# Kernel tuning notes

Measured on AMD Instinct MI355X. Metric: run time of the kernel, lower is better.

The kernel has to match this reference:

```python
import jax, jax.numpy as jnp
import numpy as np

B, N, C, H, E, K = 2, 2048, 1024, 4096, 8, 2
TAU = 1.0


def setup_inputs() -> dict:
    key = jax.random.key(0)
    ks = jax.random.split(key, 9)
    x = jax.random.normal(ks[0], (B, N, C), dtype=jnp.float32)
    T = B * N
    u = jax.random.uniform(ks[1], (T, E), minval=1e-6, maxval=1.0 - 1e-6)
    gumbel_noise = -jnp.log(-jnp.log(u))  # Gumbel(0,1) samples
    s = 0.02
    gate_w = jax.random.normal(ks[2], (C, E), dtype=jnp.float32) * s
    gate_b = jnp.zeros((E,), dtype=jnp.float32)
    w1 = jax.random.normal(ks[3], (E, C, H), dtype=jnp.float32) * s
    b1 = jnp.zeros((E, H), dtype=jnp.float32)
    w2 = jax.random.normal(ks[4], (E, H, C), dtype=jnp.float32) * s
    b2 = jnp.zeros((E, C), dtype=jnp.float32)
    return {"x": x, "gumbel_noise": gumbel_noise, "gate_w": gate_w,
            "gate_b": gate_b, "w1": w1, "b1": b1, "w2": w2, "b2": b2}


def reference(x, gumbel_noise, gate_w, gate_b, w1, b1, w2, b2):
    Bb, Nn, Cc = x.shape
    x_flat = x.reshape(-1, Cc)                                  # [T, C]
    logits = x_flat @ gate_w + gate_b                           # [T, E]
    # F.gumbel_softmax(hard=False, tau=1): softmax((logits + g)/tau)
    gates = jax.nn.softmax((logits + gumbel_noise) / TAU, axis=-1)
    mean_gates = gates.mean(axis=0)
    load_balance_loss = jnp.sum(mean_gates * jnp.log(mean_gates + 1e-8))
    topk_vals, topk_idxs = jax.lax.top_k(gates, K)              # [T, K]
    T = x_flat.shape[0]
    # scatter top-k gate weights into a dense [T, E] combine matrix
    comb = jnp.zeros((T, E), dtype=gates.dtype)
    comb = comb.at[jnp.arange(T)[:, None], topk_idxs].set(topk_vals)
    # dense per-expert MLP over all tokens, then weighted combine
    h = jnp.einsum('tc,ech->teh', x_flat, w1) + b1              # [T, E, H]
    h = jax.nn.gelu(h, approximate=False)                        # exact GELU (nn.GELU)
    y = jnp.einsum('teh,ehc->tec', h, w2) + b2                  # [T, E, C]
    out = jnp.einsum('te,tec->tc', comb, y)                     # [T, C]
    return out.reshape(Bb, Nn, Cc), load_balance_loss
```

## Files before the change

### kernel.cpp

```cpp
#include <hip/hip_runtime.h>
#include <math.h>

#define TT  4096
#define CC  1024
#define HH  4096
#define EE  8
#define TKN 8192

typedef _Float16 f16x8 __attribute__((ext_vector_type(8)));
typedef float    f32x4 __attribute__((ext_vector_type(4)));

#define GLD_LDS16(g, l)                                                        \
    __builtin_amdgcn_global_load_lds(                                          \
        (const __attribute__((address_space(1))) void*)(g),                    \
        (__attribute__((address_space(3))) void*)(l), 16, 0, 0)

__global__ __launch_bounds__(256) void gate_kernel(
    const float* __restrict__ x, const float* __restrict__ gn,
    const float* __restrict__ gw, const float* __restrict__ gb,
    int* __restrict__ topk_idx, float* __restrict__ topk_w,
    int* __restrict__ counts, float* __restrict__ gsum)
{
    int wave = threadIdx.x >> 6, lane = threadIdx.x & 63;
    int t = blockIdx.x * 4 + wave;
    const float* xrow = x + (size_t)t * CC;

    double acc[EE];
#pragma unroll
    for (int e = 0; e < EE; e++) acc[e] = 0.0;

#pragma unroll
    for (int i = 0; i < CC / 64; i++) {
        int c = i * 64 + lane;
        float xv = xrow[c];
        const float4* g4 = reinterpret_cast<const float4*>(gw + (size_t)c * EE);
        float4 g0 = g4[0], g1 = g4[1];
        double xd = (double)xv;
        acc[0] += xd * (double)g0.x; acc[1] += xd * (double)g0.y;
        acc[2] += xd * (double)g0.z; acc[3] += xd * (double)g0.w;
        acc[4] += xd * (double)g1.x; acc[5] += xd * (double)g1.y;
        acc[6] += xd * (double)g1.z; acc[7] += xd * (double)g1.w;
    }
#pragma unroll
    for (int e = 0; e < EE; e++)
#pragma unroll
        for (int off = 32; off > 0; off >>= 1)
            acc[e] += __shfl_xor(acc[e], off);

    double z[EE], m = -1e300;
#pragma unroll
    for (int e = 0; e < EE; e++) {
        z[e] = acc[e] + (double)gb[e] + (double)gn[(size_t)t * EE + e];
        m = fmax(m, z[e]);
    }
    double p[EE], s = 0.0;
#pragma unroll
    for (int e = 0; e < EE; e++) { p[e] = exp(z[e] - m); s += p[e]; }
    double inv = 1.0 / s;
    double g[EE];
#pragma unroll
    for (int e = 0; e < EE; e++) g[e] = p[e] * inv;

    int i1 = 0; double v1 = g[0];
#pragma unroll
    for (int e = 1; e < EE; e++) if (g[e] > v1) { v1 = g[e]; i1 = e; }
    int i2 = -1; double v2 = -1.0;
#pragma unroll
    for (int e = 0; e < EE; e++) if (e != i1 && g[e] > v2) { v2 = g[e]; i2 = e; }

    if (lane == 0) {
        topk_idx[t * 2 + 0] = i1; topk_w[t * 2 + 0] = (float)v1;
        topk_idx[t * 2 + 1] = i2; topk_w[t * 2 + 1] = (float)v2;
        atomicAdd(&counts[i1], 1);
        atomicAdd(&counts[i2], 1);
    }

    __shared__ float gp[4][EE];
    if (lane == 0) {
#pragma unroll
        for (int e = 0; e < EE; e++) gp[wave][e] = (float)g[e];
    }
    __syncthreads();
    if (threadIdx.x < EE) {
        float s4 = gp[0][threadIdx.x] + gp[1][threadIdx.x] +
                   gp[2][threadIdx.x] + gp[3][threadIdx.x];
        atomicAdd(&gsum[threadIdx.x], s4);
    }
}

__global__ __launch_bounds__(256) void transpose_f16_kernel(
    const float* __restrict__ src, _Float16* __restrict__ dst, int R, int Ccols)
{
    __shared__ float tile[64][65];
    int e = blockIdx.z;
    const float* s = src + (size_t)e * R * Ccols;
    _Float16* d = dst + (size_t)e * R * Ccols;
    int c0 = blockIdx.x * 64, r0 = blockIdx.y * 64;
    int tid = threadIdx.x;

    int lr = tid >> 4;
    int lc = (tid & 15) * 4;
#pragma unroll
    for (int i = 0; i < 4; i++) {
        int r = lr + i * 16;
        float4 v = *reinterpret_cast<const float4*>(
            s + (size_t)(r0 + r) * Ccols + c0 + lc);
        tile[r][lc + 0] = v.x; tile[r][lc + 1] = v.y;
        tile[r][lc + 2] = v.z; tile[r][lc + 3] = v.w;
    }
    __syncthreads();

    int oc = tid >> 2;
    int orr = (tid & 3) * 16;
    f16x8 o0, o1;
#pragma unroll
    for (int j = 0; j < 8; j++) o0[j] = (_Float16)tile[orr + j][oc];
#pragma unroll
    for (int j = 0; j < 8; j++) o1[j] = (_Float16)tile[orr + 8 + j][oc];
    *reinterpret_cast<f16x8*>(d + (size_t)(c0 + oc) * R + r0 + orr)     = o0;
    *reinterpret_cast<f16x8*>(d + (size_t)(c0 + oc) * R + r0 + orr + 8) = o1;
}

__global__ void scan_kernel(const int* __restrict__ counts, int* __restrict__ offsets,
                            const float* __restrict__ gsum, float* __restrict__ loss_out)
{
    if (threadIdx.x == 0) {
        int o = 0;
#pragma unroll
        for (int e = 0; e < EE; e++) { offsets[e] = o; o += counts[e]; }
        offsets[EE] = o;
        float L = 0.f;
#pragma unroll
        for (int e = 0; e < EE; e++) {
            float me = gsum[e] / (float)TT;
            L += me * logf(me + 1e-8f);
        }
        *loss_out = L;
    }
}

__global__ __launch_bounds__(256) void scatter_kernel(
    const int* __restrict__ topk_idx, const int* __restrict__ offsets,
    int* __restrict__ fill, int* __restrict__ rowtok, int* __restrict__ posmap)
{
    int t = blockIdx.x * 256 + threadIdx.x;
#pragma unroll
    for (int k = 0; k < 2; k++) {
        int e = topk_idx[t * 2 + k];
        int pos = offsets[e] + atomicAdd(&fill[e], 1);
        rowtok[pos] = t;
        posmap[t * 2 + k] = pos;
    }
}

__global__ __launch_bounds__(256) void gather_kernel(
    const float* __restrict__ x, const int* __restrict__ rowtok,
    _Float16* __restrict__ xg)
{
    int p = blockIdx.x * 2 + (threadIdx.x >> 7);
    int c = (threadIdx.x & 127) * 8;
    int t = rowtok[p];
    const float4* s = reinterpret_cast<const float4*>(x + (size_t)t * CC + c);
    float4 v0 = s[0], v1 = s[1];
    f16x8 o;
    o[0] = (_Float16)v0.x; o[1] = (_Float16)v0.y;
    o[2] = (_Float16)v0.z; o[3] = (_Float16)v0.w;
    o[4] = (_Float16)v1.x; o[5] = (_Float16)v1.y;
    o[6] = (_Float16)v1.z; o[7] = (_Float16)v1.w;
    *reinterpret_cast<f16x8*>(xg + (size_t)p * CC + c) = o;
}


__global__ __launch_bounds__(512, 2) void gemm1_kernel(
    const _Float16* __restrict__ xg, const _Float16* __restrict__ w1t,
    const float* __restrict__ b1, const int* __restrict__ offsets,
    _Float16* __restrict__ h)
{
    int GX = gridDim.x, GY = gridDim.y;
    int nwg = GX * GY * (int)gridDim.z;
    int f = blockIdx.x + GX * (blockIdx.y + GY * blockIdx.z);
    int cpx = nwg >> 3;
    f = (f & 7) * cpx + (f >> 3);
    int bx = f % GX; int tq = f / GX; int by = tq % GY; int bz = tq / GY;

    int e = bz;
    int segs = offsets[e];
    int M = offsets[e + 1] - segs;
    int m0 = bx * 256;
    if (m0 >= M) return;
    int n0 = by * 256;

    __shared__ __align__(16) _Float16 As[2][256 * 64];
    __shared__ __align__(16) _Float16 Bs[2][256 * 64];

    int tid = threadIdx.x;
    int wave = tid >> 6, lane = tid & 63;
    int wm = (wave >> 2) * 128, wn = (wave & 3) * 64;
    int lrow = lane & 15, kg = lane >> 4;
    int rx = lrow & 7;

    const _Float16* wB = w1t + (size_t)e * HH * CC;

    const _Float16* ap[4]; const _Float16* bp[4];
    int lofs[4];
#pragma unroll
    for (int j = 0; j < 4; j++) {
        int ch = j * 512 + tid;
        int row = ch >> 3, slot = ch & 7;
        int col = ((slot ^ (row & 7)) * 8);
        int rm = m0 + row; if (rm >= M) rm = M - 1;
        ap[j] = xg + (size_t)(segs + rm) * CC + col;
        bp[j] = wB + (size_t)(n0 + row) * CC + col;
        lofs[j] = ch * 8;
    }

    f32x4 acc[8][4];
#pragma unroll
    for (int i = 0; i < 8; i++)
#pragma unroll
        for (int j = 0; j < 4; j++)
#pragma unroll
            for (int q = 0; q < 4; q++) acc[i][j][q] = 0.f;

    auto STAGE = [&](int b) {
#pragma unroll
        for (int j = 0; j < 4; j++) {
            GLD_LDS16(ap[j], &As[b][0] + lofs[j]);
            GLD_LDS16(bp[j], &Bs[b][0] + lofs[j]);
            ap[j] += 64; bp[j] += 64;
        }
    };

    const int NK = CC / 64;
    STAGE(0);
    __syncthreads();
    int cur = 0;
    for (int t = 0; t < NK; ++t) {
        if (t + 1 < NK) STAGE(cur ^ 1);
        const _Float16* Ab = &As[cur][0];
        const _Float16* Bb = &Bs[cur][0];
#pragma unroll
        for (int s = 0; s < 2; s++) {
            f16x8 aF[8], bF[4];
#pragma unroll
            for (int i = 0; i < 8; i++) {
                int row = wm + i * 16 + lrow;
                aF[i] = *reinterpret_cast<const f16x8*>(
                    Ab + row * 64 + (((s * 4 + kg) ^ rx) * 8));
            }
#pragma unroll
            for (int j = 0; j < 4; j++) {
                int row = wn + j * 16 + lrow;
                bF[j] = *reinterpret_cast<const f16x8*>(
                    Bb + row * 64 + (((s * 4 + kg) ^ rx) * 8));
            }
            __builtin_amdgcn_s_setprio(1);
#pragma unroll
            for (int i = 0; i < 8; i++)
#pragma unroll
                for (int j = 0; j < 4; j++)
                    acc[i][j] = __builtin_amdgcn_mfma_f32_16x16x32_f16(
                        aF[i], bF[j], acc[i][j], 0, 0, 0);
            __builtin_amdgcn_s_setprio(0);
        }
        __syncthreads();
        cur ^= 1;
    }

    int rbase = (lane >> 4) * 4;
#pragma unroll
    for (int mi = 0; mi < 8; mi++) {
#pragma unroll
        for (int ni = 0; ni < 4; ni++) {
            int gcol = n0 + wn + ni * 16 + lrow;
            float bias = b1[(size_t)e * HH + gcol];
#pragma unroll
            for (int q = 0; q < 4; q++) {
                int rowl = m0 + wm + mi * 16 + rbase + q;
                if (rowl < M) {
                    float v = acc[mi][ni][q] + bias;
                    v = 0.5f * v * (1.0f + erff(v * 0.70710678118654752f));
                    h[(size_t)(segs + rowl) * HH + gcol] = (_Float16)v;
                }
            }
        }
    }
}

__global__ __launch_bounds__(512, 2) void gemm2_kernel(
    const _Float16* __restrict__ h, const _Float16* __restrict__ w2t,
    const float* __restrict__ b2, const int* __restrict__ offsets,
    float* __restrict__ y)
{
    int GX = gridDim.x, GY = gridDim.y;
    int nwg = GX * GY * (int)gridDim.z;
    int f = blockIdx.x + GX * (blockIdx.y + GY * blockIdx.z);
    int cpx = nwg >> 3;
    f = (f & 7) * cpx + (f >> 3);
    int bx = f % GX; int tq = f / GX; int by = tq % GY; int bz = tq / GY;

    int e = bz;
    int segs = offsets[e];
    int M = offsets[e + 1] - segs;
    int m0 = bx * 256;
    if (m0 >= M) return;
    int kz = by >> 2;
    int n0 = (by & 3) * 256;
    int kbeg = kz * (HH / 2);

    __shared__ __align__(16) _Float16 As[2][256 * 64];
    __shared__ __align__(16) _Float16 Bs[2][256 * 64];

    int tid = threadIdx.x;
    int wave = tid >> 6, lane = tid & 63;
    int wm = (wave >> 2) * 128, wn = (wave & 3) * 64;
    int lrow = lane & 15, kg = lane >> 4;
    int rx = lrow & 7;

    const _Float16* wB = w2t + (size_t)e * CC * HH;

    const _Float16* ap[4]; const _Float16* bp[4];
    int lofs[4];
#pragma unroll
    for (int j = 0; j < 4; j++) {
        int ch = j * 512 + tid;
        int row = ch >> 3, slot = ch & 7;
        int col = ((slot ^ (row & 7)) * 8);
        int rm = m0 + row; if (rm >= M) rm = M - 1;
        ap[j] = h  + (size_t)(segs + rm) * HH + kbeg + col;
        bp[j] = wB + (size_t)(n0 + row) * HH + kbeg + col;
        lofs[j] = ch * 8;
    }

    f32x4 acc[8][4];
#pragma unroll
    for (int i = 0; i < 8; i++)
#pragma unroll
        for (int j = 0; j < 4; j++)
#pragma unroll
            for (int q = 0; q < 4; q++) acc[i][j][q] = 0.f;

    auto STAGE = [&](int b) {
#pragma unroll
        for (int j = 0; j < 4; j++) {
            GLD_LDS16(ap[j], &As[b][0] + lofs[j]);
            GLD_LDS16(bp[j], &Bs[b][0] + lofs[j]);
            ap[j] += 64; bp[j] += 64;
        }
    };

    const int NK = (HH / 2) / 64;
    STAGE(0);
    __syncthreads();
    int cur = 0;
    for (int t = 0; t < NK; ++t) {
        if (t + 1 < NK) STAGE(cur ^ 1);
        const _Float16* Ab = &As[cur][0];
        const _Float16* Bb = &Bs[cur][0];
#pragma unroll
        for (int s = 0; s < 2; s++) {
            f16x8 aF[8], bF[4];
#pragma unroll
            for (int i = 0; i < 8; i++) {
                int row = wm + i * 16 + lrow;
                aF[i] = *reinterpret_cast<const f16x8*>(
                    Ab + row * 64 + (((s * 4 + kg) ^ rx) * 8));
            }
#pragma unroll
            for (int j = 0; j < 4; j++) {
                int row = wn + j * 16 + lrow;
                bF[j] = *reinterpret_cast<const f16x8*>(
                    Bb + row * 64 + (((s * 4 + kg) ^ rx) * 8));
            }
            __builtin_amdgcn_s_setprio(1);
#pragma unroll
            for (int i = 0; i < 8; i++)
#pragma unroll
                for (int j = 0; j < 4; j++)
                    acc[i][j] = __builtin_amdgcn_mfma_f32_16x16x32_f16(
                        aF[i], bF[j], acc[i][j], 0, 0, 0);
            __builtin_amdgcn_s_setprio(0);
        }
        __syncthreads();
        cur ^= 1;
    }

    float* yk = y + (size_t)kz * TKN * CC;
    int rbase = (lane >> 4) * 4;
#pragma unroll
    for (int mi = 0; mi < 8; mi++) {
#pragma unroll
        for (int ni = 0; ni < 4; ni++) {
            int gcol = n0 + wn + ni * 16 + lrow;
            float bias = (kz == 0) ? b2[(size_t)e * CC + gcol] : 0.f;
#pragma unroll
            for (int q = 0; q < 4; q++) {
                int rowl = m0 + wm + mi * 16 + rbase + q;
                if (rowl < M)
                    yk[(size_t)(segs + rowl) * CC + gcol] = acc[mi][ni][q] + bias;
            }
        }
    }
}

__global__ __launch_bounds__(256) void combine_kernel(
    const float* __restrict__ y, const int* __restrict__ posmap,
    const float* __restrict__ topk_w, float* __restrict__ out)
{
    int t = blockIdx.x * 2 + (threadIdx.x >> 7);
    int c = (threadIdx.x & 127) * 8;
    int p0 = posmap[t * 2 + 0], p1 = posmap[t * 2 + 1];
    float wa = topk_w[t * 2 + 0], wb = topk_w[t * 2 + 1];
    const float* y1 = y + (size_t)TKN * CC;
    const float4* a0 = reinterpret_cast<const float4*>(y  + (size_t)p0 * CC + c);
    const float4* a1 = reinterpret_cast<const float4*>(y1 + (size_t)p0 * CC + c);
    const float4* b0 = reinterpret_cast<const float4*>(y  + (size_t)p1 * CC + c);
    const float4* b1 = reinterpret_cast<const float4*>(y1 + (size_t)p1 * CC + c);
    float4 r0, r1;
    float4 av0 = a0[0], av1 = a0[1], aw0 = a1[0], aw1 = a1[1];
    float4 bv0 = b0[0], bv1 = b0[1], bw0 = b1[0], bw1 = b1[1];
    r0.x = wa * (av0.x + aw0.x) + wb * (bv0.x + bw0.x);
    r0.y = wa * (av0.y + aw0.y) + wb * (bv0.y + bw0.y);
    r0.z = wa * (av0.z + aw0.z) + wb * (bv0.z + bw0.z);
    r0.w = wa * (av0.w + aw0.w) + wb * (bv0.w + bw0.w);
    r1.x = wa * (av1.x + aw1.x) + wb * (bv1.x + bw1.x);
    r1.y = wa * (av1.y + aw1.y) + wb * (bv1.y + bw1.y);
    r1.z = wa * (av1.z + aw1.z) + wb * (bv1.z + bw1.z);
    r1.w = wa * (av1.w + aw1.w) + wb * (bv1.w + bw1.w);
    float4* o = reinterpret_cast<float4*>(out + (size_t)t * CC + c);
    o[0] = r0; o[1] = r1;
}

extern "C" void kernel_launch(void* const* d_in, const int* in_sizes, int n_in,
                              void* d_out, int out_size, void* d_ws, size_t ws_size,
                              hipStream_t stream)
{
    const float* x  = (const float*)d_in[0];
    const float* gn = (const float*)d_in[1];
    const float* gw = (const float*)d_in[2];
    const float* gb = (const float*)d_in[3];
    const float* w1 = (const float*)d_in[4];
    const float* b1 = (const float*)d_in[5];
    const float* w2 = (const float*)d_in[6];
    const float* b2 = (const float*)d_in[7];
    float* out = (float*)d_out;

    char* w = (char*)d_ws;
    int*   counts  = (int*)(w + 0);
    int*   fill    = (int*)(w + 32);
    int*   offsets = (int*)(w + 64);
    float* gsum    = (float*)(w + 128);
    size_t off = 256;
    int*   topk_idx = (int*)(w + off);   off += (size_t)TT * 2 * 4;
    float* topk_w   = (float*)(w + off); off += (size_t)TT * 2 * 4;
    int*   rowtok   = (int*)(w + off);   off += (size_t)TKN * 4;
    int*   posmap   = (int*)(w + off);   off += (size_t)TKN * 4;
    _Float16* xg  = (_Float16*)(w + off); off += (size_t)TKN * CC * 2;
    _Float16* w1t = (_Float16*)(w + off); off += (size_t)EE * HH * CC * 2;
    _Float16* w2t = (_Float16*)(w + off); off += (size_t)EE * CC * HH * 2;
    _Float16* hbuf = (_Float16*)(w + off); off += (size_t)TKN * HH * 2;
    float* ybuf = (float*)w1t;

    (void)hipMemsetAsync(d_ws, 0, 256, stream);

    gate_kernel<<<TT / 4, 256, 0, stream>>>(x, gn, gw, gb, topk_idx, topk_w,
                                            counts, gsum);
    transpose_f16_kernel<<<dim3(HH / 64, CC / 64, EE), 256, 0, stream>>>(
        w1, w1t, CC, HH);
    transpose_f16_kernel<<<dim3(CC / 64, HH / 64, EE), 256, 0, stream>>>(
        w2, w2t, HH, CC);
    scan_kernel<<<1, 64, 0, stream>>>(counts, offsets, gsum, out + (size_t)TT * CC);
    scatter_kernel<<<TT / 256, 256, 0, stream>>>(topk_idx, offsets, fill,
                                                 rowtok, posmap);
    gather_kernel<<<TKN / 2, 256, 0, stream>>>(x, rowtok, xg);
    gemm1_kernel<<<dim3(6, HH / 256, EE), 512, 0, stream>>>(xg, w1t, b1,
                                                            offsets, hbuf);
    gemm2_kernel<<<dim3(6, 2 * (CC / 256), EE), 512, 0, stream>>>(
        hbuf, w2t, b2, offsets, ybuf);
    combine_kernel<<<TT / 2, 256, 0, stream>>>(ybuf, posmap, topk_w, out);
}
```

Baseline: 848.1 us.

## Shrink GEMM tiles to 128x128, drop gemm2 split-K, fuse weight transposes

Both expert GEMMs move from 256x256 tiles with 512 threads to 128x128 tiles with 256 threads. The grid is doubled in M so it still covers the largest expert, which improves load balance across ragged expert sizes. Gemm2 drops its 2-way split-K, so the combine kernel reads one y buffer instead of summing two partial buffers. The two weight transpose launches become a single kernel in which each block handles four 64x64 tiles, loading the next tile while storing the current one. Smaller tiles lower arithmetic intensity and increase global and LDS traffic per FLOP.

Measured after the change: 882.8 us. 4.1% more time.

```diff
diff --git a/kernel.cpp b/kernel.cpp
--- a/kernel.cpp
+++ b/kernel.cpp
@@ -88,37 +88,63 @@
     }
 }
 
-__global__ __launch_bounds__(256) void transpose_f16_kernel(
-    const float* __restrict__ src, _Float16* __restrict__ dst, int R, int Ccols)
-{
-    __shared__ float tile[64][65];
-    int e = blockIdx.z;
-    const float* s = src + (size_t)e * R * Ccols;
-    _Float16* d = dst + (size_t)e * R * Ccols;
-    int c0 = blockIdx.x * 64, r0 = blockIdx.y * 64;
+__global__ __launch_bounds__(256) void transpose_both_kernel(
+    const float* __restrict__ w1, _Float16* __restrict__ w1t,
+    const float* __restrict__ w2, _Float16* __restrict__ w2t)
+{
+    __shared__ float tile[2][64][65];
+    int idx = blockIdx.x;
+    const float* src; _Float16* dst; int R, Cc, localn;
+    if (idx < 2048) { src = w1; dst = w1t; R = CC; Cc = HH; localn = idx; }
+    else            { src = w2; dst = w2t; R = HH; Cc = CC; localn = idx - 2048; }
+    int e = localn >> 8;
+    int rem = localn & 255;
+    int ctiles = Cc >> 8;
+    int ct = rem % ctiles, rt = rem / ctiles;
+    int c0 = ct * 256, r0 = rt * 64;
+    src += (size_t)e * R * Cc;
+    dst += (size_t)e * R * Cc;
+
     int tid = threadIdx.x;
-
     int lr = tid >> 4;
     int lc = (tid & 15) * 4;
-#pragma unroll
-    for (int i = 0; i < 4; i++) {
-        int r = lr + i * 16;
-        float4 v = *reinterpret_cast<const float4*>(
-            s + (size_t)(r0 + r) * Ccols + c0 + lc);
-        tile[r][lc + 0] = v.x; tile[r][lc + 1] = v.y;
-        tile[r][lc + 2] = v.z; tile[r][lc + 3] = v.w;
-    }
-    __syncthreads();
-
     int oc = tid >> 2;
     int orr = (tid & 3) * 16;
-    f16x8 o0, o1;
-#pragma unroll
-    for (int j = 0; j < 8; j++) o0[j] = (_Float16)tile[orr + j][oc];
-#pragma unroll
-    for (int j = 0; j < 8; j++) o1[j] = (_Float16)tile[orr + 8 + j][oc];
-    *reinterpret_cast<f16x8*>(d + (size_t)(c0 + oc) * R + r0 + orr)     = o0;
-    *reinterpret_cast<f16x8*>(d + (size_t)(c0 + oc) * R + r0 + orr + 8) = o1;
+
+    float4 v[4];
+    auto GLOAD = [&](int t) {
+#pragma unroll
+        for (int i = 0; i < 4; i++)
+            v[i] = *reinterpret_cast<const float4*>(
+                src + (size_t)(r0 + lr + i * 16) * Cc + c0 + t * 64 + lc);
+    };
+    auto LWRITE = [&](int b) {
+#pragma unroll
+        for (int i = 0; i < 4; i++) {
+            tile[b][lr + i * 16][lc + 0] = v[i].x;
+            tile[b][lr + i * 16][lc + 1] = v[i].y;
+            tile[b][lr + i * 16][lc + 2] = v[i].z;
+            tile[b][lr + i * 16][lc + 3] = v[i].w;
+        }
+    };
+    auto STORE = [&](int t, int b) {
+        f16x8 o0, o1;
+#pragma unroll
+        for (int j = 0; j < 8; j++) o0[j] = (_Float16)tile[b][orr + j][oc];
+#pragma unroll
+        for (int j = 0; j < 8; j++) o1[j] = (_Float16)tile[b][orr + 8 + j][oc];
+        _Float16* dp = dst + (size_t)(c0 + t * 64 + oc) * R + r0 + orr;
+        *reinterpret_cast<f16x8*>(dp)     = o0;
+        *reinterpret_cast<f16x8*>(dp + 8) = o1;
+    };
+
+    GLOAD(0); LWRITE(0);
+    for (int t = 0; t < 4; ++t) {
+        __syncthreads();
+        if (t < 3) GLOAD(t + 1);
+        STORE(t, t & 1);
+        if (t < 3) LWRITE((t + 1) & 1);
+    }
 }
 
 __global__ void scan_kernel(const int* __restrict__ counts, int* __restrict__ offsets,
@@ -171,7 +197,7 @@
 }
 
 
-__global__ __launch_bounds__(512, 2) void gemm1_kernel(
+__global__ __launch_bounds__(256, 2) void gemm1_kernel(
     const _Float16* __restrict__ xg, const _Float16* __restrict__ w1t,
     const float* __restrict__ b1, const int* __restrict__ offsets,
     _Float16* __restrict__ h)
@@ -186,16 +212,16 @@
     int e = bz;
     int segs = offsets[e];
     int M = offsets[e + 1] - segs;
-    int m0 = bx * 256;
+    int m0 = bx * 128;
     if (m0 >= M) return;
-    int n0 = by * 256;
-
-    __shared__ __align__(16) _Float16 As[2][256 * 64];
-    __shared__ __align__(16) _Float16 Bs[2][256 * 64];
+    int n0 = by * 128;
+
+    __shared__ __align__(16) _Float16 As[2][128 * 64];
+    __shared__ __align__(16) _Float16 Bs[2][128 * 64];
 
     int tid = threadIdx.x;
     int wave = tid >> 6, lane = tid & 63;
-    int wm = (wave >> 2) * 128, wn = (wave & 3) * 64;
+    int wm = (wave >> 1) * 64, wn = (wave & 1) * 64;
     int lrow = lane & 15, kg = lane >> 4;
     int rx = lrow & 7;
 
@@ -205,18 +231,18 @@
     int lofs[4];
 #pragma unroll
     for (int j = 0; j < 4; j++) {
-        int ch = j * 512 + tid;
+        int ch = j * 256 + tid;
         int row = ch >> 3, slot = ch & 7;
-        int col = ((slot ^ (row & 7)) * 8);
+        int col = (slot ^ (row & 7)) * 8;
         int rm = m0 + row; if (rm >= M) rm = M - 1;
         ap[j] = xg + (size_t)(segs + rm) * CC + col;
         bp[j] = wB + (size_t)(n0 + row) * CC + col;
         lofs[j] = ch * 8;
     }
 
-    f32x4 acc[8][4];
-#pragma unroll
-    for (int i = 0; i < 8; i++)
+    f32x4 acc[4][4];
+#pragma unroll
+    for (int i = 0; i < 4; i++)
 #pragma unroll
         for (int j = 0; j < 4; j++)
 #pragma unroll
@@ -241,9 +267,9 @@
         const _Float16* Bb = &Bs[cur][0];
 #pragma unroll
         for (int s = 0; s < 2; s++) {
-            f16x8 aF[8], bF[4];
-#pragma unroll
-            for (int i = 0; i < 8; i++) {
+            f16x8 aF[4], bF[4];
+#pragma unroll
+            for (int i = 0; i < 4; i++) {
                 int row = wm + i * 16 + lrow;
                 aF[i] = *reinterpret_cast<const f16x8*>(
                     Ab + row * 64 + (((s * 4 + kg) ^ rx) * 8));
@@ -256,7 +282,7 @@
             }
             __builtin_amdgcn_s_setprio(1);
 #pragma unroll
-            for (int i = 0; i < 8; i++)
+            for (int i = 0; i < 4; i++)
 #pragma unroll
                 for (int j = 0; j < 4; j++)
                     acc[i][j] = __builtin_amdgcn_mfma_f32_16x16x32_f16(
@@ -269,7 +295,7 @@
 
     int rbase = (lane >> 4) * 4;
 #pragma unroll
-    for (int mi = 0; mi < 8; mi++) {
+    for (int mi = 0; mi < 4; mi++) {
 #pragma unroll
         for (int ni = 0; ni < 4; ni++) {
             int gcol = n0 + wn + ni * 16 + lrow;
@@ -287,7 +313,7 @@
     }
 }
 
-__global__ __launch_bounds__(512, 2) void gemm2_kernel(
+__global__ __launch_bounds__(256, 2) void gemm2_kernel(
     const _Float16* __restrict__ h, const _Float16* __restrict__ w2t,
     const float* __restrict__ b2, const int* __restrict__ offsets,
     float* __restrict__ y)
@@ -302,18 +328,16 @@
     int e = bz;
     int segs = offsets[e];
     int M = offsets[e + 1] - segs;
-    int m0 = bx * 256;
+    int m0 = bx * 128;
     if (m0 >= M) return;
-    int kz = by >> 2;
-    int n0 = (by & 3) * 256;
-    int kbeg = kz * (HH / 2);
-
-    __shared__ __align__(16) _Float16 As[2][256 * 64];
-    __shared__ __align__(16) _Float16 Bs[2][256 * 64];
+    int n0 = by * 128;
+
+    __shared__ __align__(16) _Float16 As[2][128 * 64];
+    __shared__ __align__(16) _Float16 Bs[2][128 * 64];
 
     int tid = threadIdx.x;
     int wave = tid >> 6, lane = tid & 63;
-    int wm = (wave >> 2) * 128, wn = (wave & 3) * 64;
+    int wm = (wave >> 1) * 64, wn = (wave & 1) * 64;
     int lrow = lane & 15, kg = lane >> 4;
     int rx = lrow & 7;
 
@@ -323,18 +347,18 @@
     int lofs[4];
 #pragma unroll
     for (int j = 0; j < 4; j++) {
-        int ch = j * 512 + tid;
+        int ch = j * 256 + tid;
         int row = ch >> 3, slot = ch & 7;
-        int col = ((slot ^ (row & 7)) * 8);
+        int col = (slot ^ (row & 7)) * 8;
         int rm = m0 + row; if (rm >= M) rm = M - 1;
-        ap[j] = h  + (size_t)(segs + rm) * HH + kbeg + col;
-        bp[j] = wB + (size_t)(n0 + row) * HH + kbeg + col;
+        ap[j] = h  + (size_t)(segs + rm) * HH + col;
+        bp[j] = wB + (size_t)(n0 + row) * HH + col;
         lofs[j] = ch * 8;
     }
 
-    f32x4 acc[8][4];
-#pragma unroll
-    for (int i = 0; i < 8; i++)
+    f32x4 acc[4][4];
+#pragma unroll
+    for (int i = 0; i < 4; i++)
 #pragma unroll
         for (int j = 0; j < 4; j++)
 #pragma unroll
@@ -349,7 +373,7 @@
         }
     };
 
-    const int NK = (HH / 2) / 64;
+    const int NK = HH / 64;
     STAGE(0);
     __syncthreads();
     int cur = 0;
@@ -359,9 +383,9 @@
         const _Float16* Bb = &Bs[cur][0];
 #pragma unroll
         for (int s = 0; s < 2; s++) {
-            f16x8 aF[8], bF[4];
-#pragma unroll
-            for (int i = 0; i < 8; i++) {
+            f16x8 aF[4], bF[4];
+#pragma unroll
+            for (int i = 0; i < 4; i++) {
                 int row = wm + i * 16 + lrow;
                 aF[i] = *reinterpret_cast<const f16x8*>(
                     Ab + row * 64 + (((s * 4 + kg) ^ rx) * 8));
@@ -374,7 +398,7 @@
             }
             __builtin_amdgcn_s_setprio(1);
 #pragma unroll
-            for (int i = 0; i < 8; i++)
+            for (int i = 0; i < 4; i++)
 #pragma unroll
                 for (int j = 0; j < 4; j++)
                     acc[i][j] = __builtin_amdgcn_mfma_f32_16x16x32_f16(
@@ -385,19 +409,18 @@
         cur ^= 1;
     }
 
-    float* yk = y + (size_t)kz * TKN * CC;
     int rbase = (lane >> 4) * 4;
 #pragma unroll
-    for (int mi = 0; mi < 8; mi++) {
+    for (int mi = 0; mi < 4; mi++) {
 #pragma unroll
         for (int ni = 0; ni < 4; ni++) {
             int gcol = n0 + wn + ni * 16 + lrow;
-            float bias = (kz == 0) ? b2[(size_t)e * CC + gcol] : 0.f;
+            float bias = b2[(size_t)e * CC + gcol];
 #pragma unroll
             for (int q = 0; q < 4; q++) {
                 int rowl = m0 + wm + mi * 16 + rbase + q;
                 if (rowl < M)
-                    yk[(size_t)(segs + rowl) * CC + gcol] = acc[mi][ni][q] + bias;
+                    y[(size_t)(segs + rowl) * CC + gcol] = acc[mi][ni][q] + bias;
             }
         }
     }
@@ -411,22 +434,14 @@
     int c = (threadIdx.x & 127) * 8;
     int p0 = posmap[t * 2 + 0], p1 = posmap[t * 2 + 1];
     float wa = topk_w[t * 2 + 0], wb = topk_w[t * 2 + 1];
-    const float* y1 = y + (size_t)TKN * CC;
-    const float4* a0 = reinterpret_cast<const float4*>(y  + (size_t)p0 * CC + c);
-    const float4* a1 = reinterpret_cast<const float4*>(y1 + (size_t)p0 * CC + c);
-    const float4* b0 = reinterpret_cast<const float4*>(y  + (size_t)p1 * CC + c);
-    const float4* b1 = reinterpret_cast<const float4*>(y1 + (size_t)p1 * CC + c);
+    const float4* a = reinterpret_cast<const float4*>(y + (size_t)p0 * CC + c);
+    const float4* b = reinterpret_cast<const float4*>(y + (size_t)p1 * CC + c);
+    float4 a0 = a[0], a1 = a[1], b0 = b[0], b1 = b[1];
     float4 r0, r1;
-    float4 av0 = a0[0], av1 = a0[1], aw0 = a1[0], aw1 = a1[1];
-    float4 bv0 = b0[0], bv1 = b0[1], bw0 = b1[0], bw1 = b1[1];
-    r0.x = wa * (av0.x + aw0.x) + wb * (bv0.x + bw0.x);
-    r0.y = wa * (av0.y + aw0.y) + wb * (bv0.y + bw0.y);
-    r0.z = wa * (av0.z + aw0.z) + wb * (bv0.z + bw0.z);
-    r0.w = wa * (av0.w + aw0.w) + wb * (bv0.w + bw0.w);
-    r1.x = wa * (av1.x + aw1.x) + wb * (bv1.x + bw1.x);
-    r1.y = wa * (av1.y + aw1.y) + wb * (bv1.y + bw1.y);
-    r1.z = wa * (av1.z + aw1.z) + wb * (bv1.z + bw1.z);
-    r1.w = wa * (av1.w + aw1.w) + wb * (bv1.w + bw1.w);
+    r0.x = wa * a0.x + wb * b0.x; r0.y = wa * a0.y + wb * b0.y;
+    r0.z = wa * a0.z + wb * b0.z; r0.w = wa * a0.w + wb * b0.w;
+    r1.x = wa * a1.x + wb * b1.x; r1.y = wa * a1.y + wb * b1.y;
+    r1.z = wa * a1.z + wb * b1.z; r1.w = wa * a1.w + wb * b1.w;
     float4* o = reinterpret_cast<float4*>(out + (size_t)t * CC + c);
     o[0] = r0; o[1] = r1;
 }
@@ -465,17 +480,14 @@
 
     gate_kernel<<<TT / 4, 256, 0, stream>>>(x, gn, gw, gb, topk_idx, topk_w,
                                             counts, gsum);
-    transpose_f16_kernel<<<dim3(HH / 64, CC / 64, EE), 256, 0, stream>>>(
-        w1, w1t, CC, HH);
-    transpose_f16_kernel<<<dim3(CC / 64, HH / 64, EE), 256, 0, stream>>>(
-        w2, w2t, HH, CC);
+    transpose_both_kernel<<<4096, 256, 0, stream>>>(w1, w1t, w2, w2t);
     scan_kernel<<<1, 64, 0, stream>>>(counts, offsets, gsum, out + (size_t)TT * CC);
     scatter_kernel<<<TT / 256, 256, 0, stream>>>(topk_idx, offsets, fill,
                                                  rowtok, posmap);
     gather_kernel<<<TKN / 2, 256, 0, stream>>>(x, rowtok, xg);
-    gemm1_kernel<<<dim3(6, HH / 256, EE), 512, 0, stream>>>(xg, w1t, b1,
-                                                            offsets, hbuf);
-    gemm2_kernel<<<dim3(6, 2 * (CC / 256), EE), 512, 0, stream>>>(
+    gemm1_kernel<<<dim3(12, HH / 128, EE), 256, 0, stream>>>(xg, w1t, b1,
+                                                             offsets, hbuf);
+    gemm2_kernel<<<dim3(12, CC / 128, EE), 256, 0, stream>>>(
         hbuf, w2t, b2, offsets, ybuf);
     combine_kernel<<<TT / 2, 256, 0, stream>>>(ybuf, posmap, topk_w, out);
 }
```
